# Optimization experiments

Measured on AMD Instinct MI355X. Metric: run time of the kernel, lower is better.

The kernel has to match this reference:

```python
import jax, jax.numpy as jnp
import numpy as np

G_DOWNSAMPLED = 16  # g_downsampled_dimension: tiling factor
XF_DIM = 1024       # xf_dimension
BATCH = 2048


def setup_inputs() -> dict:
    key = jax.random.key(0)
    k1, k2 = jax.random.split(key)
    xf = jax.random.normal(k1, (BATCH, XF_DIM), dtype=jnp.float32)
    wp = jax.random.normal(k2, (1,), dtype=jnp.float32)
    return {"xf": xf, "wp": wp}


def reference(xf, wp):
    # xf_r = relu(xf - mean_batch(xf))
    xf_r = jax.nn.relu(xf - jnp.mean(xf, axis=0))
    # fn_xf = (xf_r - mean(xf_r)) / std(xf_r), std unbiased (torch default ddof=1)
    mu = jnp.mean(xf_r, axis=0)
    sd = jnp.std(xf_r, axis=0, ddof=1)
    fn_xf = (xf_r - mu) / sd
    # matmul with W_tile = kron(ones(1,g), eye(xf_dim)) is an exact tile along features
    x_ = wp * jnp.tile(fn_xf, (1, G_DOWNSAMPLED))  # [batch, g*xf_dim]
    return x_
```

## Files before the change

### kernel.cpp

```cpp
#include <hip/hip_runtime.h>

#define BATCH 2048
#define FDIM  1024
#define GTILE 16
#define F4    (FDIM / 4)
#define CHUNKS 256
#define ROWS_PER_CHUNK (BATCH / CHUNKS)

#define OFF_P1   0
#define OFF_MEAN 262144
#define OFF_SC   263168
#define OFF_CC   264192

__device__ __forceinline__ void v4add(float4& a, const float4& b) {
    a.x += b.x; a.y += b.y; a.z += b.z; a.w += b.w;
}

__global__ void k1_partial_sum(const float4* __restrict__ xf, float4* __restrict__ p1) {
    const int tid = threadIdx.x;
    const int chunk = blockIdx.x;
    const float4* p = xf + (size_t)chunk * ROWS_PER_CHUNK * F4 + tid;
    float4 s = {0.f, 0.f, 0.f, 0.f};
#pragma unroll
    for (int r = 0; r < ROWS_PER_CHUNK; ++r) v4add(s, p[r * F4]);
    p1[chunk * F4 + tid] = s;
}

__global__ void k23_stats(const float4* __restrict__ xf,
                          const float* __restrict__ wp,
                          const float4* __restrict__ p1,
                          float4* __restrict__ mean,
                          float4* __restrict__ sc,
                          float4* __restrict__ cc) {
    __shared__ float4 rA[256], rB[256];
    const int t = threadIdx.x;
    const int b = blockIdx.x;

    rA[t] = p1[t * F4 + b];
    __syncthreads();
    for (int off = 128; off > 0; off >>= 1) {
        if (t < off) v4add(rA[t], rA[t + off]);
        __syncthreads();
    }
    const float inv_n = 1.0f / (float)BATCH;
    float4 m = rA[0];
    m.x *= inv_n; m.y *= inv_n; m.z *= inv_n; m.w *= inv_n;
    if (t == 0) mean[b] = m;

    const float4* p = xf + (size_t)t * ROWS_PER_CHUNK * F4 + b;
    float4 s = {0.f, 0.f, 0.f, 0.f};
    float4 q = {0.f, 0.f, 0.f, 0.f};
#pragma unroll
    for (int r = 0; r < ROWS_PER_CHUNK; ++r) {
        float4 v = p[r * F4];
        float rx = fmaxf(v.x - m.x, 0.f);
        float ry = fmaxf(v.y - m.y, 0.f);
        float rz = fmaxf(v.z - m.z, 0.f);
        float rw = fmaxf(v.w - m.w, 0.f);
        s.x += rx; s.y += ry; s.z += rz; s.w += rw;
        q.x += rx * rx; q.y += ry * ry; q.z += rz * rz; q.w += rw * rw;
    }
    __syncthreads();
    rA[t] = s; rB[t] = q;
    __syncthreads();
    for (int off = 128; off > 0; off >>= 1) {
        if (t < off) { v4add(rA[t], rA[t + off]); v4add(rB[t], rB[t + off]); }
        __syncthreads();
    }
    if (t == 0) {
        const float w = wp[0];
        float4 S = rA[0], Q = rB[0];
        float4 scale, cmb;
        float mu, var;
        mu = S.x * inv_n; var = (Q.x - S.x * mu) / (float)(BATCH - 1);
        scale.x = w * rsqrtf(var); cmb.x = mu * scale.x;
        mu = S.y * inv_n; var = (Q.y - S.y * mu) / (float)(BATCH - 1);
        scale.y = w * rsqrtf(var); cmb.y = mu * scale.y;
        mu = S.z * inv_n; var = (Q.z - S.z * mu) / (float)(BATCH - 1);
        scale.z = w * rsqrtf(var); cmb.z = mu * scale.z;
        mu = S.w * inv_n; var = (Q.w - S.w * mu) / (float)(BATCH - 1);
        scale.w = w * rsqrtf(var); cmb.w = mu * scale.w;
        sc[b] = scale;
        cc[b] = cmb;
    }
}

__global__ void k4_write(const float4* __restrict__ xf,
                         const float4* __restrict__ mean,
                         const float4* __restrict__ sc,
                         const float4* __restrict__ cc,
                         float4* __restrict__ out) {
    const int tid = threadIdx.x;
    const int row = blockIdx.x;
    float4 m = mean[tid];
    float4 a = sc[tid];
    float4 c = cc[tid];
    float4 v = xf[(size_t)row * F4 + tid];
    float4 o;
    o.x = fmaxf(v.x - m.x, 0.f) * a.x - c.x;
    o.y = fmaxf(v.y - m.y, 0.f) * a.y - c.y;
    o.z = fmaxf(v.z - m.z, 0.f) * a.z - c.z;
    o.w = fmaxf(v.w - m.w, 0.f) * a.w - c.w;
    float4* dst = out + (size_t)row * (GTILE * F4) + tid;
#pragma unroll
    for (int g = 0; g < GTILE; ++g) {
        dst[g * F4] = o;
    }
}

extern "C" void kernel_launch(void* const* d_in, const int* in_sizes, int n_in,
                              void* d_out, int out_size, void* d_ws, size_t ws_size,
                              hipStream_t stream) {
    const float4* xf4 = (const float4*)d_in[0];
    const float* wp = (const float*)d_in[1];
    float* ws = (float*)d_ws;
    float4* out = (float4*)d_out;

    float4* p1   = (float4*)(ws + OFF_P1);
    float4* mean = (float4*)(ws + OFF_MEAN);
    float4* sc   = (float4*)(ws + OFF_SC);
    float4* cc   = (float4*)(ws + OFF_CC);

    k1_partial_sum<<<CHUNKS, 256, 0, stream>>>(xf4, p1);
    k23_stats<<<F4, 256, 0, stream>>>(xf4, wp, p1, mean, sc, cc);
    k4_write<<<BATCH, 256, 0, stream>>>(xf4, mean, sc, cc, out);
}
```

Measured before the change: 157.8 us.

## Restructure stats pass to coalesced row-chunk blocks with atomic accumulation

The second stats kernel changes from one block per feature-group (256 blocks each reading strided rows) to one block per row chunk that reads contiguous rows. Each block redundantly reduces the 128 partial sums to get the mean, then adds its relu sum and square sum into global accumulators with float atomics. A last-block counter computes scale and offset. Chunk count drops to 128, giving fewer blocks with more rows each. This aims for coalesced loads and removes the shared-memory tree reductions, at the cost of atomic contention and nondeterministic float summation order.

```diff
diff --git a/kernel.cpp b/kernel.cpp
--- a/kernel.cpp
+++ b/kernel.cpp
@@ -4,21 +4,33 @@
 #define FDIM  1024
 #define GTILE 16
 #define F4    (FDIM / 4)
-#define CHUNKS 256
+#define CHUNKS 128
 #define ROWS_PER_CHUNK (BATCH / CHUNKS)
 
 #define OFF_P1   0
-#define OFF_MEAN 262144
-#define OFF_SC   263168
-#define OFF_CC   264192
+#define OFF_SACC 131072
+#define OFF_QACC 132096
+#define OFF_MEAN 133120
+#define OFF_SC   134144
+#define OFF_CC   135168
+#define OFF_CNT  136192
 
 __device__ __forceinline__ void v4add(float4& a, const float4& b) {
     a.x += b.x; a.y += b.y; a.z += b.z; a.w += b.w;
 }
 
-__global__ void k1_partial_sum(const float4* __restrict__ xf, float4* __restrict__ p1) {
+__global__ void k1_partial_sum(const float4* __restrict__ xf,
+                               float4* __restrict__ p1,
+                               float* __restrict__ sacc,
+                               float* __restrict__ qacc,
+                               int* __restrict__ counter) {
     const int tid = threadIdx.x;
     const int chunk = blockIdx.x;
+    if (chunk == 0) {
+        sacc[tid] = 0.f; sacc[tid + 256] = 0.f; sacc[tid + 512] = 0.f; sacc[tid + 768] = 0.f;
+        qacc[tid] = 0.f; qacc[tid + 256] = 0.f; qacc[tid + 512] = 0.f; qacc[tid + 768] = 0.f;
+        if (tid == 0) *counter = 0;
+    }
     const float4* p = xf + (size_t)chunk * ROWS_PER_CHUNK * F4 + tid;
     float4 s = {0.f, 0.f, 0.f, 0.f};
 #pragma unroll
@@ -26,28 +38,26 @@
     p1[chunk * F4 + tid] = s;
 }
 
-__global__ void k23_stats(const float4* __restrict__ xf,
-                          const float* __restrict__ wp,
-                          const float4* __restrict__ p1,
-                          float4* __restrict__ mean,
-                          float4* __restrict__ sc,
-                          float4* __restrict__ cc) {
-    __shared__ float4 rA[256], rB[256];
-    const int t = threadIdx.x;
-    const int b = blockIdx.x;
+__global__ void k2_relu_stats(const float4* __restrict__ xf,
+                              const float* __restrict__ wp,
+                              const float4* __restrict__ p1,
+                              float* __restrict__ sacc,
+                              float* __restrict__ qacc,
+                              float4* __restrict__ mean,
+                              float4* __restrict__ sc,
+                              float4* __restrict__ cc,
+                              int* __restrict__ counter) {
+    const int tid = threadIdx.x;
+    const int chunk = blockIdx.x;
+    __shared__ int isLast;
 
-    rA[t] = p1[t * F4 + b];
-    __syncthreads();
-    for (int off = 128; off > 0; off >>= 1) {
-        if (t < off) v4add(rA[t], rA[t + off]);
-        __syncthreads();
-    }
+    float4 m = {0.f, 0.f, 0.f, 0.f};
+#pragma unroll 8
+    for (int c = 0; c < CHUNKS; ++c) v4add(m, p1[c * F4 + tid]);
     const float inv_n = 1.0f / (float)BATCH;
-    float4 m = rA[0];
     m.x *= inv_n; m.y *= inv_n; m.z *= inv_n; m.w *= inv_n;
-    if (t == 0) mean[b] = m;
 
-    const float4* p = xf + (size_t)t * ROWS_PER_CHUNK * F4 + b;
+    const float4* p = xf + (size_t)chunk * ROWS_PER_CHUNK * F4 + tid;
     float4 s = {0.f, 0.f, 0.f, 0.f};
     float4 q = {0.f, 0.f, 0.f, 0.f};
 #pragma unroll
@@ -60,29 +70,40 @@
         s.x += rx; s.y += ry; s.z += rz; s.w += rw;
         q.x += rx * rx; q.y += ry * ry; q.z += rz * rz; q.w += rw * rw;
     }
+    atomicAdd(&sacc[tid * 4 + 0], s.x); atomicAdd(&sacc[tid * 4 + 1], s.y);
+    atomicAdd(&sacc[tid * 4 + 2], s.z); atomicAdd(&sacc[tid * 4 + 3], s.w);
+    atomicAdd(&qacc[tid * 4 + 0], q.x); atomicAdd(&qacc[tid * 4 + 1], q.y);
+    atomicAdd(&qacc[tid * 4 + 2], q.z); atomicAdd(&qacc[tid * 4 + 3], q.w);
+
+    __threadfence();
     __syncthreads();
-    rA[t] = s; rB[t] = q;
+    if (tid == 0) {
+        int old = atomicAdd(counter, 1);
+        isLast = (old == CHUNKS - 1);
+    }
     __syncthreads();
-    for (int off = 128; off > 0; off >>= 1) {
-        if (t < off) { v4add(rA[t], rA[t + off]); v4add(rB[t], rB[t + off]); }
-        __syncthreads();
-    }
-    if (t == 0) {
-        const float w = wp[0];
-        float4 S = rA[0], Q = rB[0];
-        float4 scale, cmb;
-        float mu, var;
-        mu = S.x * inv_n; var = (Q.x - S.x * mu) / (float)(BATCH - 1);
-        scale.x = w * rsqrtf(var); cmb.x = mu * scale.x;
-        mu = S.y * inv_n; var = (Q.y - S.y * mu) / (float)(BATCH - 1);
-        scale.y = w * rsqrtf(var); cmb.y = mu * scale.y;
-        mu = S.z * inv_n; var = (Q.z - S.z * mu) / (float)(BATCH - 1);
-        scale.z = w * rsqrtf(var); cmb.z = mu * scale.z;
-        mu = S.w * inv_n; var = (Q.w - S.w * mu) / (float)(BATCH - 1);
-        scale.w = w * rsqrtf(var); cmb.w = mu * scale.w;
-        sc[b] = scale;
-        cc[b] = cmb;
-    }
+    if (!isLast) return;
+    __threadfence();
+
+    float4 S, Q;
+    S.x = sacc[tid * 4 + 0]; S.y = sacc[tid * 4 + 1];
+    S.z = sacc[tid * 4 + 2]; S.w = sacc[tid * 4 + 3];
+    Q.x = qacc[tid * 4 + 0]; Q.y = qacc[tid * 4 + 1];
+    Q.z = qacc[tid * 4 + 2]; Q.w = qacc[tid * 4 + 3];
+    const float w = wp[0];
+    float4 scale, cmb;
+    float mu, var;
+    mu = S.x * inv_n; var = (Q.x - S.x * mu) / (float)(BATCH - 1);
+    scale.x = w * rsqrtf(var); cmb.x = mu * scale.x;
+    mu = S.y * inv_n; var = (Q.y - S.y * mu) / (float)(BATCH - 1);
+    scale.y = w * rsqrtf(var); cmb.y = mu * scale.y;
+    mu = S.z * inv_n; var = (Q.z - S.z * mu) / (float)(BATCH - 1);
+    scale.z = w * rsqrtf(var); cmb.z = mu * scale.z;
+    mu = S.w * inv_n; var = (Q.w - S.w * mu) / (float)(BATCH - 1);
+    scale.w = w * rsqrtf(var); cmb.w = mu * scale.w;
+    mean[tid] = m;
+    sc[tid]   = scale;
+    cc[tid]   = cmb;
 }
 
 __global__ void k4_write(const float4* __restrict__ xf,
@@ -117,11 +138,14 @@
     float4* out = (float4*)d_out;
 
     float4* p1   = (float4*)(ws + OFF_P1);
+    float* sacc  = ws + OFF_SACC;
+    float* qacc  = ws + OFF_QACC;
     float4* mean = (float4*)(ws + OFF_MEAN);
     float4* sc   = (float4*)(ws + OFF_SC);
     float4* cc   = (float4*)(ws + OFF_CC);
+    int* counter = (int*)(ws + OFF_CNT);
 
-    k1_partial_sum<<<CHUNKS, 256, 0, stream>>>(xf4, p1);
-    k23_stats<<<F4, 256, 0, stream>>>(xf4, wp, p1, mean, sc, cc);
+    k1_partial_sum<<<CHUNKS, 256, 0, stream>>>(xf4, p1, sacc, qacc, counter);
+    k2_relu_stats<<<CHUNKS, 256, 0, stream>>>(xf4, wp, p1, sacc, qacc, mean, sc, cc, counter);
     k4_write<<<BATCH, 256, 0, stream>>>(xf4, mean, sc, cc, out);
 }
```

Measured after the change: 170.6 us. +8.1%, slower.
